# Kernel tuning notes

Hardware: AMD Instinct MI355X
Metric: run time of the kernel (lower is better)

The kernel has to match this reference:

```python
import jax, jax.numpy as jnp
import numpy as np

D_MODEL = 1024
NHEAD = 16
HEAD_DIM = D_MODEL // NHEAD
SCALE = 1.0 / np.sqrt(HEAD_DIM).astype(np.float32)
B, L = 2, 2048
NEG_INF = -1e30


def setup_inputs() -> dict:
    key = jax.random.key(0)
    ks = jax.random.split(key, 12)
    xav = np.sqrt(6.0 / (D_MODEL + D_MODEL)).astype(np.float32)  # xavier_uniform gain=1
    def lin_w(k):
        return jax.random.uniform(k, (D_MODEL, D_MODEL), jnp.float32, -xav, xav)
    x = jax.random.normal(ks[0], (B, L, D_MODEL), jnp.float32)
    role_mask = jax.random.randint(ks[1], (B, L), 0, 2, jnp.int32)
    # causal attention mask: True = masked (upper triangle above diagonal)
    attn_mask = jnp.triu(jnp.ones((L, L), jnp.bool_), k=1)
    # random key padding: True = padded key
    key_padding_mask = jax.random.randint(ks[2], (B, L), 0, 2, jnp.int32).astype(jnp.bool_)
    return {
        "x": x,
        "role_mask": role_mask,
        "attn_mask": attn_mask,
        "key_padding_mask": key_padding_mask,
        "Wq": lin_w(ks[3]), "bq": jnp.zeros((D_MODEL,), jnp.float32),
        "Wk": lin_w(ks[4]), "bk": jnp.zeros((D_MODEL,), jnp.float32),
        "Wv": lin_w(ks[5]), "bv": jnp.zeros((D_MODEL,), jnp.float32),
        "Wo": lin_w(ks[6]), "bo": jnp.zeros((D_MODEL,), jnp.float32),
        "delta": jnp.asarray(1.0, jnp.float32),
    }


def reference(x, role_mask, attn_mask, key_padding_mask,
              Wq, bq, Wk, bk, Wv, bv, Wo, bo, delta):
    Bb, Ll, Dd = x.shape
    def heads(t):  # [B,L,D] -> [B,H,L,hd]
        return t.reshape(Bb, Ll, NHEAD, HEAD_DIM).transpose(0, 2, 1, 3)
    Q = heads(x @ Wq.T + bq)
    K = heads(x @ Wk.T + bk)
    V = heads(x @ Wv.T + bv)
    scores = jnp.einsum('bhqd,bhkd->bhqk', Q, K) * SCALE  # [B,H,L,L]
    same_role = (role_mask[:, :, None] == role_mask[:, None, :])  # [B,L,L]
    scores = scores + (same_role.astype(scores.dtype) * delta)[:, None, :, :]
    scores = jnp.where(attn_mask[None, None, :, :], -jnp.inf, scores)
    scores = jnp.where(key_padding_mask[:, None, None, :], -jnp.inf, scores)
    attn = jax.nn.softmax(scores, axis=-1)
    attn = jnp.nan_to_num(attn, nan=0.0, posinf=0.0, neginf=0.0)
    out = jnp.einsum('bhqk,bhkd->bhqd', attn, V)
    out = out.transpose(0, 2, 1, 3).reshape(Bb, Ll, Dd)
    return out @ Wo.T + bo
```

## Files before the change

### kernel.cpp

```cpp
#include <hip/hip_runtime.h>
#include <hip/hip_bf16.h>

#define DM 1024
#define NH 16
#define HD 64
#define BB 2
#define LL 2048
#define BL (BB * LL)
#define SCALE 0.125f
#define NEG_BIG -1e30f
#define LOG2E 1.4426950408889634f
#define SC2 (SCALE * LOG2E)
#define FIXM 16.0f
#define SLOTB 8448
#define POOL0_SLOTS 960

typedef __bf16 bf16;
typedef __bf16 bf16x8 __attribute__((ext_vector_type(8)));
typedef __bf16 bf16x4 __attribute__((ext_vector_type(4)));
typedef float f32x4 __attribute__((ext_vector_type(4)));

static __device__ inline bf16x8 load8(const bf16* p) {
    return *reinterpret_cast<const bf16x8*>(p);
}

static __device__ inline float scrub(float x) {
    union { float f; unsigned u; } c; c.f = x;
    return ((c.u & 0x7F800000u) == 0x7F800000u) ? 0.f : x;
}

typedef __attribute__((address_space(1))) const unsigned char ga_t;
typedef __attribute__((address_space(3))) unsigned char ls_t;
static __device__ inline void gload_lds16(const void* g, void* l) {
    __builtin_amdgcn_global_load_lds((ga_t*)g, (ls_t*)l, 16, 0, 0);
}

__global__ __launch_bounds__(256) void prep_all(
    const float* __restrict__ x,
    const float* __restrict__ Wq, const float* __restrict__ Wk,
    const float* __restrict__ Wv, const float* __restrict__ Wo,
    bf16* __restrict__ xb, bf16* __restrict__ Wqb, bf16* __restrict__ Wkb,
    bf16* __restrict__ Wvb, bf16* __restrict__ Wob,
    const int* __restrict__ role, const void* __restrict__ kpad,
    const float* __restrict__ deltap,
    float* __restrict__ biasC, int* __restrict__ cntq, int* __restrict__ ipos,
    bf16* __restrict__ kwc)
{
    const int tid = threadIdx.x;
    const int gid = blockIdx.x;
    if (gid < 2048) {
        const float* src; bf16* dst; size_t base;
        if (gid < 1024) { src = x; dst = xb; base = (size_t)gid * 1024; }
        else {
            const int wsel = (gid - 1024) >> 8;
            src = (wsel == 0) ? Wq : (wsel == 1) ? Wk : (wsel == 2) ? Wv : Wo;
            dst = (wsel == 0) ? Wqb : (wsel == 1) ? Wkb : (wsel == 2) ? Wvb : Wob;
            base = (size_t)((gid - 1024) & 255) * 1024;
        }
#pragma unroll
        for (int it = 0; it < 4; it++) {
            const size_t i = base + it * 256 + tid;
            const f32x4 v = ((const f32x4*)src)[i];
            bf16x4 o;
            o[0] = (bf16)v[0]; o[1] = (bf16)v[1]; o[2] = (bf16)v[2]; o[3] = (bf16)v[3];
            ((bf16x4*)dst)[i] = o;
        }
        return;
    }
    const int b = gid - 2048;
    const unsigned char* kb = (const unsigned char*)kpad;
    int f3F = 0, fLow = 0, fOff = 0;
    for (int i = (tid & 63); i < BL; i += 64) {
        const unsigned char v = kb[i];
        if (v == 0x3F) f3F = 1;
        if ((i & 3) < 2 && v) fLow = 1;
        if ((i & 3) && v) fOff = 1;
    }
    const int mode = __any(f3F) ? (__any(fLow) ? 3 : 2) : (__any(fOff) ? 1 : 0);

    __shared__ int ssum[256];
    int loc[8]; int s = 0;
#pragma unroll
    for (int j = 0; j < 8; j++) {
        const int i = tid * 8 + j, idx = b * LL + i;
        const bool pad = (mode == 0) ? (((const int*)kpad)[idx] != 0)
                       : (mode == 1) ? (((const unsigned char*)kpad)[idx] != 0)
                       : (mode == 2) ? (((const float*)kpad)[idx] != 0.f)
                                     : (((const unsigned short*)kpad)[idx] != 0);
        loc[j] = pad ? 0 : 1; s += loc[j];
    }
    ssum[tid] = s; __syncthreads();
    for (int off = 1; off < 256; off <<= 1) {
        const int t = (tid >= off) ? ssum[tid - off] : 0;
        __syncthreads();
        ssum[tid] += t;
        __syncthreads();
    }
    const int nv = ssum[255];
    int run = ssum[tid] - s;
    const float d2 = scrub(deltap[0]) * LOG2E;
#pragma unroll
    for (int j = 0; j < 8; j++) {
        const int i = tid * 8 + j, idx = b * LL + i;
        const int inc = run + loc[j];
        cntq[idx] = inc;
        if (loc[j]) {
            const int cp = inc - 1;
            const int r = role[idx];
            biasC[b * LL + cp]      = -FIXM + ((r == 0) ? d2 : 0.f);
            biasC[BL + b * LL + cp] = -FIXM + ((r == 1) ? d2 : 0.f);
            ipos[b * LL + cp] = i;
        }
        run = inc;
    }
    for (int i = nv + tid; i < LL; i += 256) {
        biasC[b * LL + i] = NEG_BIG;
        biasC[BL + b * LL + i] = NEG_BIG;
    }
    const int roundv = (nv + 63) & ~63;
    const int nt = roundv - nv;
    bf16x8 z;
#pragma unroll
    for (int j = 0; j < 8; j++) z[j] = (bf16)0.f;
    for (int u = tid; u < nt * NH * 8; u += 256) {
        const int c8 = u & 7; const int t2 = u >> 3;
        const int h = t2 / nt; const int rr = nv + t2 % nt;
        *(bf16x8*)&kwc[(((size_t)(b * NH + h) * LL) + rr) * HD + c8 * 8] = z;
    }
}

__global__ __launch_bounds__(256) void qkv_bf16(
    const bf16* __restrict__ xb,
    const bf16* __restrict__ Wqb, const bf16* __restrict__ Wkb, const bf16* __restrict__ Wvb,
    const float* __restrict__ bq, const float* __restrict__ bk, const float* __restrict__ bv,
    bf16* __restrict__ qw, bf16* __restrict__ kwc, bf16* __restrict__ vwc,
    const int* __restrict__ ipos, const int* __restrict__ cntq)
{
    __shared__ bf16 As[2][128 * 32];
    __shared__ bf16 Bs[2][128 * 32];
    const int tid = threadIdx.x;
    const int lane = tid & 63, w = tid >> 6;
    const int wm = w >> 1, wn = w & 1;
    const int ln = lane & 15, quad = lane >> 4;

    const int lin = blockIdx.y * 32 + blockIdx.x;
    const int xcd = lin & 7;
    const int t = lin >> 3;
    const int mloc = t & 3;
    const int yy = t >> 2;
    const int mt = xcd * 4 + mloc;
    const int sel = yy >> 3;
    const int nloc0 = (yy & 7) * 128;

    int b = 0, cp0 = 0, nvb = 0, m0 = 0;
    if (sel == 0) {
        m0 = mt * 128;
    } else {
        b = mt >> 4;
        cp0 = (mt & 15) * 128;
        nvb = cntq[b * LL + LL - 1];
        if (cp0 >= nvb) return;
    }

    const bf16* Wb = (sel == 0) ? Wqb : ((sel == 1) ? Wkb : Wvb);
    const float* bias = (sel == 0) ? bq : ((sel == 1) ? bk : bv);
    bf16* dstw = (sel == 0) ? qw : ((sel == 1) ? kwc : vwc);

    const int rA = lane >> 2;
    const int cA = (lane & 3) * 8;

    const bf16* asrc[2];
    const bf16* bsrc[2];
#pragma unroll
    for (int s = 0; s < 2; s++) {
        const int r = s * 64 + w * 16 + rA;
        int grow;
        if (sel == 0) grow = m0 + r;
        else {
            const int cp = cp0 + r;
            grow = b * LL + ((cp < nvb) ? ipos[b * LL + cp] : 0);
        }
        asrc[s] = xb + (size_t)grow * DM + cA;
        bsrc[s] = Wb + (size_t)(nloc0 + s * 64 + w * 16 + rA) * DM + cA;
    }

#pragma unroll
    for (int s = 0; s < 2; s++) {
        const int r0 = s * 64 + w * 16;
        gload_lds16(asrc[s], &As[0][r0 * 32]);
        gload_lds16(bsrc[s], &Bs[0][r0 * 32]);
    }

    f32x4 acc[4][4] = {};
    int cur = 0;
    for (int k0 = 0; k0 < DM; k0 += 32) {
        if (k0 + 32 < DM) {
#pragma unroll
            for (int s = 0; s < 2; s++) {
                const int r0 = s * 64 + w * 16;
                gload_lds16(asrc[s] + k0 + 32, &As[cur ^ 1][r0 * 32]);
                gload_lds16(bsrc[s] + k0 + 32, &Bs[cur ^ 1][r0 * 32]);
            }
            asm volatile("s_waitcnt vmcnt(4)" ::: "memory");
        } else {
            asm volatile("s_waitcnt vmcnt(0)" ::: "memory");
        }
        __builtin_amdgcn_s_barrier();

        bf16x8 a[4], bfr[4];
#pragma unroll
        for (int mi = 0; mi < 4; mi++)
            a[mi] = *(bf16x8*)&As[cur][(wm * 64 + mi * 16 + ln) * 32 + quad * 8];
#pragma unroll
        for (int ni = 0; ni < 4; ni++)
            bfr[ni] = *(bf16x8*)&Bs[cur][(wn * 64 + ni * 16 + ln) * 32 + quad * 8];
#pragma unroll
        for (int mi = 0; mi < 4; mi++)
#pragma unroll
            for (int ni = 0; ni < 4; ni++)
                acc[mi][ni] = __builtin_amdgcn_mfma_f32_16x16x32_bf16(a[mi], bfr[ni], acc[mi][ni], 0, 0, 0);

        __builtin_amdgcn_s_barrier();
        cur ^= 1;
    }

#pragma unroll
    for (int mi = 0; mi < 4; mi++) {
#pragma unroll
        for (int i = 0; i < 4; i++) {
            const int rr = wm * 64 + mi * 16 + quad * 4 + i;
            int batch, drow; bool valid;
            if (sel == 0) {
                const int row = m0 + rr;
                batch = row >> 11; drow = row & (LL - 1); valid = true;
            } else {
                const int cp = cp0 + rr;
                batch = b; drow = cp; valid = (cp < nvb);
            }
#pragma unroll
            for (int ni = 0; ni < 4; ni++) {
                const int ncol = nloc0 + wn * 64 + ni * 16 + ln;
                const int hh = ncol >> 6, dd = ncol & 63;
                const bf16 v = (bf16)scrub(acc[mi][ni][i] + bias[ncol]);
                if (valid)
                    dstw[(((size_t)(batch * NH + hh) * LL) + drow) * HD + dd] = v;
            }
        }
    }
}

__global__ __launch_bounds__(256) void vtrans(
    const bf16* __restrict__ vwc, bf16* __restrict__ vtc, const int* __restrict__ cntq)
{
    __shared__ bf16 T[64][72];
    const int l0 = blockIdx.x * 64;
    const int bh = blockIdx.y;
    const int b = bh >> 4;
    const int nv = cntq[b * LL + LL - 1];
    if (l0 >= ((nv + 63) & ~63)) return;
    const int tid = threadIdx.x;
#pragma unroll
    for (int it = 0; it < 2; it++) {
        const int idx = it * 256 + tid;
        const int row = idx >> 3, c8 = (idx & 7) * 8;
        const int wc = (((c8 >> 3) ^ ((row >> 3) & 7))) * 8;
        bf16x8 val;
#pragma unroll
        for (int j = 0; j < 8; j++) val[j] = (bf16)0.f;
        if (l0 + row < nv) val = load8(vwc + ((size_t)bh * LL + l0 + row) * HD + c8);
        *(bf16x8*)&T[row][wc] = val;
    }
    __syncthreads();
#pragma unroll
    for (int it = 0; it < 2; it++) {
        const int idx = it * 256 + tid;
        const int dd = idx >> 3, pg = (idx & 7) * 8;
        bf16x8 o;
#pragma unroll
        for (int j = 0; j < 8; j++) {
            const int r = pg + j;
            o[j] = T[r][(dd & 7) + ((((dd >> 3) ^ ((r >> 3) & 7))) << 3)];
        }
        *(bf16x8*)(vtc + ((size_t)bh * HD + dd) * LL + l0 + pg) = o;
    }
}

__global__ __launch_bounds__(256) void attn_v14(
    const bf16* __restrict__ qw, const bf16* __restrict__ kwc, const bf16* __restrict__ vtc,
    const int* __restrict__ role, const float* __restrict__ biasC, const int* __restrict__ cntq,
    char* __restrict__ pool0, char* __restrict__ pool1,
    bf16* __restrict__ attn_out)
{
    const int lin = blockIdx.y * 60 + blockIdx.x;
    const int xcd = lin & 7;
    const int t = lin >> 3;
    const int xg = t % 60;
    const int g = t / 60;
    const int bh = g * 8 + xcd;

    int qb, c;
    if (xg < 24)      { qb = 31 - xg / 3; c = xg % 3; }
    else if (xg < 48) { qb = 23 - (xg - 24) / 2; c = (xg - 24) % 2; }
    else              { qb = 59 - xg; c = 0; }
    const int nch = (qb + 12) / 12;

    __shared__ bf16 Ks[2][2][64 * 32];
    __shared__ bf16 Vs[2][2][64 * 32];

    const int tid = threadIdx.x;
    const int lane = tid & 63, w = tid >> 6;
    const int col = lane & 15, quad = lane >> 4;
    const int h = bh & (NH - 1), b = bh >> 4;
    const int q0 = qb * 64 + w * 16;

    const bf16* qbase = qw + (size_t)((b * NH + h) * LL) * HD;
    const bf16* kbase = kwc + (size_t)((b * NH + h) * LL) * HD;
    const bf16* vbase = vtc + (size_t)((b * NH + h) * HD) * LL;
    const int* rrow = role + b * LL;

    const int srow = lane >> 2;
    const int sslot = w * 16 + srow;
    const int trueK = ((sslot >> 5) & 1) * 32 + ((sslot >> 2) & 3) * 8
                    + ((sslot >> 4) & 1) * 4 + (sslot & 3);
    const int swz = ((lane & 3) ^ ((lane >> 3) & 3)) * 8;
    const bf16* ksrc = kbase + (size_t)trueK * HD + swz;
    const bf16* vsrc = vbase + (size_t)(w * 16 + srow) * LL + swz;

    bf16x8 qf[2];
    qf[0] = load8(qbase + (size_t)(q0 + col) * HD + quad * 8);
    qf[1] = load8(qbase + (size_t)(q0 + col) * HD + 32 + quad * 8);

    bf16x8 ones;
#pragma unroll
    for (int j = 0; j < 8; j++) ones[j] = (bf16)1.0f;

    const int qabs = q0 + col;
    const int role_q = rrow[qabs];
    const int cnt_q = cntq[b * LL + qabs];
    const float* bp = biasC + (size_t)role_q * BL + b * LL;

    const int cb = cntq[b * LL + qb * 64 + 63];
    const int Tb = (cb + 63) >> 6;
    const int t0c = (c * Tb) / nch;
    const int t1c = ((c + 1) * Tb) / nch;

    f32x4 ol = {};
    f32x4 o[4] = {};

    if (t0c < t1c) {
        const int kp = t0c * 64;
#pragma unroll
        for (int st = 0; st < 2; st++)
            gload_lds16(ksrc + (size_t)kp * HD + st * 32, &Ks[0][st][w * 512]);
#pragma unroll
        for (int kh = 0; kh < 2; kh++)
            gload_lds16(vsrc + kp + kh * 32, &Vs[0][kh][w * 512]);
    }

    const int rs = (quad ^ ((col >> 1) & 3)) * 8;

    for (int kt = t0c; kt < t1c; kt++) {
        const int cur = (kt - t0c) & 1;
        __syncthreads();

        if (kt + 1 < t1c) {
            const int k1 = (kt + 1) * 64;
#pragma unroll
            for (int st = 0; st < 2; st++)
                gload_lds16(ksrc + (size_t)k1 * HD + st * 32, &Ks[cur ^ 1][st][w * 512]);
#pragma unroll
            for (int kh = 0; kh < 2; kh++)
                gload_lds16(vsrc + k1 + kh * 32, &Vs[cur ^ 1][kh][w * 512]);
        }

        const int k0 = kt * 64;

        f32x4 s[4] = {};
#pragma unroll
        for (int st = 0; st < 2; st++) {
#pragma unroll
            for (int ns = 0; ns < 4; ns++) {
                const bf16x8 kf = *(bf16x8*)&Ks[cur][st][(ns * 16 + col) * 32 + rs];
                s[ns] = __builtin_amdgcn_mfma_f32_16x16x32_bf16(kf, qf[st], s[ns], 0, 0, 0);
            }
        }

        bf16x8 pf[2];
#pragma unroll
        for (int ns = 0; ns < 4; ns++) {
            const int kb_ = k0 + ((ns >> 1) << 5) + (quad << 3) + ((ns & 1) << 2);
            const f32x4 bv4 = *(const f32x4*)&bp[kb_];
#pragma unroll
            for (int i = 0; i < 4; i++) {
                float sv = fmaf(s[ns][i], SC2, bv4[i]);
                if ((kb_ + i) >= cnt_q) sv = NEG_BIG;
                pf[ns >> 1][(ns & 1) * 4 + i] = (bf16)exp2f(sv);
            }
        }

#pragma unroll
        for (int ns = 0; ns < 4; ns++) {
#pragma unroll
            for (int kh = 0; kh < 2; kh++) {
                const bf16x8 vf = *(bf16x8*)&Vs[cur][kh][(ns * 16 + col) * 32 + rs];
                o[ns] = __builtin_amdgcn_mfma_f32_16x16x32_bf16(vf, pf[kh], o[ns], 0, 0, 0);
            }
        }
#pragma unroll
        for (int kh = 0; kh < 2; kh++)
            ol = __builtin_amdgcn_mfma_f32_16x16x32_bf16(ones, pf[kh], ol, 0, 0, 0);
    }

    if (nch == 1) {
        const float inv = (ol[0] > 0.f) ? 1.f / ol[0] : 0.f;
        bf16* orow = attn_out + ((size_t)(b * LL) + qabs) * DM + h * HD;
#pragma unroll
        for (int ns = 0; ns < 4; ns++) {
            bf16x4 ov;
#pragma unroll
            for (int i = 0; i < 4; i++) ov[i] = (bf16)scrub(o[ns][i] * inv);
            *(bf16x4*)&orow[ns * 16 + quad * 4] = ov;
        }
    } else {
        const int base = (qb <= 23) ? (qb - 12) * 2 : 24 + (qb - 24) * 3;
        const int slot = bh * 48 + base + c;
        char* ptr = (slot < POOL0_SLOTS) ? (pool0 + (size_t)slot * SLOTB)
                                         : (pool1 + (size_t)(slot - POOL0_SLOTS) * SLOTB);
        bf16* op = (bf16*)ptr;
        float* lp = (float*)(ptr + 8192);
        const int r = w * 16 + col;
        if (quad == 0) lp[r] = ol[0];
#pragma unroll
        for (int ns = 0; ns < 4; ns++) {
            bf16x4 ov;
#pragma unroll
            for (int i = 0; i < 4; i++) ov[i] = (bf16)scrub(o[ns][i]);
            *(bf16x4*)&op[r * 64 + ns * 16 + quad * 4] = ov;
        }
    }
}

__global__ __launch_bounds__(256) void combine(
    const char* __restrict__ pool0, const char* __restrict__ pool1,
    bf16* __restrict__ attn_out)
{
    const int qb = 12 + blockIdx.x;
    const int bh = blockIdx.y;
    const int h = bh & (NH - 1), b = bh >> 4;
    const int nch = (qb + 12) / 12;
    const int base = (qb <= 23) ? (qb - 12) * 2 : 24 + (qb - 24) * 3;

    const char* ptr[3];
    for (int c = 0; c < nch; c++) {
        const int slot = bh * 48 + base + c;
        ptr[c] = (slot < POOL0_SLOTS) ? (pool0 + (size_t)slot * SLOTB)
                                      : (pool1 + (size_t)(slot - POOL0_SLOTS) * SLOTB);
    }

    __shared__ float linv[64];
    const int tid = threadIdx.x;
    if (tid < 64) {
        float ls = 0.f;
        for (int c = 0; c < nch; c++) ls += ((const float*)(ptr[c] + 8192))[tid];
        linv[tid] = (ls > 0.f) ? 1.f / ls : 0.f;
    }
    __syncthreads();

    const int r = tid >> 2;
    const int d0 = (tid & 3) * 16;
    float acc[16] = {};
    for (int c = 0; c < nch; c++) {
        const bf16* op = (const bf16*)ptr[c];
#pragma unroll
        for (int half = 0; half < 2; half++) {
            const bf16x8 v = load8(op + r * 64 + d0 + half * 8);
#pragma unroll
            for (int j = 0; j < 8; j++) acc[half * 8 + j] += (float)v[j];
        }
    }
    const float inv = linv[r];
    bf16x8 outv[2];
#pragma unroll
    for (int half = 0; half < 2; half++)
#pragma unroll
        for (int j = 0; j < 8; j++)
            outv[half][j] = (bf16)scrub(acc[half * 8 + j] * inv);
    bf16* orow = attn_out + ((size_t)(b * LL) + qb * 64 + r) * DM + h * HD + d0;
    *(bf16x8*)orow = outv[0];
    *(bf16x8*)(orow + 8) = outv[1];
}

__global__ __launch_bounds__(256) void out_bf16(
    const bf16* __restrict__ A, const bf16* __restrict__ Wb,
    const float* __restrict__ bias, float* __restrict__ out)
{
    __shared__ bf16 As[128 * 32];
    __shared__ bf16 Bs[64 * 32];
    const int tid = threadIdx.x;
    const int lane = tid & 63, w = tid >> 6;
    const int ln = lane & 15, quad = lane >> 4;

    const int lin = blockIdx.y * 32 + blockIdx.x;
    const int xcd = lin & 7;
    const int t = lin >> 3;
    const int mloc = t & 3;
    const int n = t >> 2;
    const int m0 = (xcd * 4 + mloc) * 128;
    const int n0 = n * 64;

    const int rA = lane >> 2;
    const int cA = (lane & 3) * 8;

    f32x4 acc[2][4] = {};
    for (int k0 = 0; k0 < DM; k0 += 32) {
        __syncthreads();
#pragma unroll
        for (int s = 0; s < 2; s++) {
            const int r0 = s * 64 + w * 16;
            gload_lds16(A + (size_t)(m0 + r0 + rA) * DM + k0 + cA, &As[r0 * 32]);
        }
        gload_lds16(Wb + (size_t)(n0 + w * 16 + rA) * DM + k0 + cA, &Bs[w * 16 * 32]);
        __syncthreads();
        bf16x8 a[2], b[4];
#pragma unroll
        for (int mi = 0; mi < 2; mi++)
            a[mi] = *(bf16x8*)&As[(w * 32 + mi * 16 + ln) * 32 + quad * 8];
#pragma unroll
        for (int ni = 0; ni < 4; ni++)
            b[ni] = *(bf16x8*)&Bs[(ni * 16 + ln) * 32 + quad * 8];
#pragma unroll
        for (int mi = 0; mi < 2; mi++)
#pragma unroll
            for (int ni = 0; ni < 4; ni++)
                acc[mi][ni] = __builtin_amdgcn_mfma_f32_16x16x32_bf16(a[mi], b[ni], acc[mi][ni], 0, 0, 0);
    }
#pragma unroll
    for (int mi = 0; mi < 2; mi++) {
#pragma unroll
        for (int ni = 0; ni < 4; ni++) {
            const int ncol = n0 + ni * 16 + ln;
            const float bv_ = bias[ncol];
#pragma unroll
            for (int i = 0; i < 4; i++) {
                const int row = m0 + w * 32 + mi * 16 + quad * 4 + i;
                out[(size_t)row * DM + ncol] = scrub(acc[mi][ni][i] + bv_);
            }
        }
    }
}

extern "C" void kernel_launch(void* const* d_in, const int* in_sizes, int n_in,
                              void* d_out, int out_size, void* d_ws, size_t ws_size,
                              hipStream_t stream) {
    const float* x    = (const float*)d_in[0];
    const int*   role = (const int*)d_in[1];
    const void*  kpad = d_in[3];
    const float* Wq = (const float*)d_in[4];
    const float* bq = (const float*)d_in[5];
    const float* Wk = (const float*)d_in[6];
    const float* bk = (const float*)d_in[7];
    const float* Wv = (const float*)d_in[8];
    const float* bv = (const float*)d_in[9];
    const float* Wo = (const float*)d_in[10];
    const float* bo = (const float*)d_in[11];
    const float* dl = (const float*)d_in[12];

    char* ws = (char*)d_ws;
    bf16* qw   = (bf16*)(ws);
    bf16* kwc  = (bf16*)(ws + (size_t)(8u  << 20));
    bf16* Wqb  = (bf16*)(ws + (size_t)(16u << 20));
    bf16* Wkb  = (bf16*)(ws + (size_t)(18u << 20));
    bf16* Wvb  = (bf16*)(ws + (size_t)(20u << 20));
    char* pool0 = ws + (size_t)(16u << 20);
    bf16* vwc  = (bf16*)(ws + (size_t)(24u << 20));
    bf16* aw   = (bf16*)(ws + (size_t)(24u << 20));
    bf16* vtc  = (bf16*)(ws + (size_t)(32u << 20));
    bf16* xb   = (bf16*)(ws + (size_t)(40u << 20));
    char* pool1 = ws + (size_t)(40u << 20);
    float* biasC = (float*)(ws + (size_t)(48u << 20));
    int*   cntq  = (int*)(ws + (size_t)(48u << 20) + 32768);
    int*   ipos  = (int*)(ws + (size_t)(48u << 20) + 49152);
    bf16* Wob  = (bf16*)(ws + (size_t)(48u << 20) + 65536);
    float* out = (float*)d_out;

    prep_all<<<dim3(2050), dim3(256), 0, stream>>>(
        x, Wq, Wk, Wv, Wo, xb, Wqb, Wkb, Wvb, Wob,
        role, kpad, dl, biasC, cntq, ipos, kwc);
    qkv_bf16<<<dim3(32, 24), dim3(256), 0, stream>>>(
        xb, Wqb, Wkb, Wvb, bq, bk, bv, qw, kwc, vwc, ipos, cntq);
    vtrans<<<dim3(32, 32), dim3(256), 0, stream>>>(vwc, vtc, cntq);
    attn_v14<<<dim3(60, 32), dim3(256), 0, stream>>>(
        qw, kwc, vtc, role, biasC, cntq, pool0, pool1, aw);
    combine<<<dim3(20, 32), dim3(256), 0, stream>>>(pool0, pool1, aw);
    out_bf16<<<dim3(32, 16), dim3(256), 0, stream>>>(aw, Wob, bo, out);
}
```

Measured before the change: 217.3 us.

## Triple-buffer LDS prefetch in QKV and output projection GEMMs

The QKV projection GEMM moves from double to triple LDS buffering with a two-stage-ahead prefetch, and its vmcnt waits are adjusted to match. The output projection GEMM, which previously loaded synchronously with two __syncthreads per k-step, gets the same three-buffer async pipeline. Sched barriers keep the compiler from reordering LDS reads across the barriers. The aim is to hide global-load latency behind MFMA work, at the cost of more LDS per block and possibly lower occupancy.

```diff
diff --git a/kernel.cpp b/kernel.cpp
--- a/kernel.cpp
+++ b/kernel.cpp
@@ -136,8 +136,8 @@
     bf16* __restrict__ qw, bf16* __restrict__ kwc, bf16* __restrict__ vwc,
     const int* __restrict__ ipos, const int* __restrict__ cntq)
 {
-    __shared__ bf16 As[2][128 * 32];
-    __shared__ bf16 Bs[2][128 * 32];
+    __shared__ bf16 As[3][128 * 32];
+    __shared__ bf16 Bs[3][128 * 32];
     const int tid = threadIdx.x;
     const int lane = tid & 63, w = tid >> 6;
     const int wm = w >> 1, wn = w & 1;
@@ -190,22 +190,33 @@
         gload_lds16(asrc[s], &As[0][r0 * 32]);
         gload_lds16(bsrc[s], &Bs[0][r0 * 32]);
     }
+#pragma unroll
+    for (int s = 0; s < 2; s++) {
+        const int r0 = s * 64 + w * 16;
+        gload_lds16(asrc[s] + 32, &As[1][r0 * 32]);
+        gload_lds16(bsrc[s] + 32, &Bs[1][r0 * 32]);
+    }
 
     f32x4 acc[4][4] = {};
     int cur = 0;
-    for (int k0 = 0; k0 < DM; k0 += 32) {
-        if (k0 + 32 < DM) {
+    for (int kk = 0; kk < 32; ++kk) {
+        if (kk + 2 < 32) {
+            const int pf = (cur >= 1) ? cur - 1 : 2;
+            const int ko = (kk + 2) * 32;
 #pragma unroll
             for (int s = 0; s < 2; s++) {
                 const int r0 = s * 64 + w * 16;
-                gload_lds16(asrc[s] + k0 + 32, &As[cur ^ 1][r0 * 32]);
-                gload_lds16(bsrc[s] + k0 + 32, &Bs[cur ^ 1][r0 * 32]);
+                gload_lds16(asrc[s] + ko, &As[pf][r0 * 32]);
+                gload_lds16(bsrc[s] + ko, &Bs[pf][r0 * 32]);
             }
+            asm volatile("s_waitcnt vmcnt(8)" ::: "memory");
+        } else if (kk + 2 == 32) {
             asm volatile("s_waitcnt vmcnt(4)" ::: "memory");
         } else {
             asm volatile("s_waitcnt vmcnt(0)" ::: "memory");
         }
         __builtin_amdgcn_s_barrier();
+        __builtin_amdgcn_sched_barrier(0);
 
         bf16x8 a[4], bfr[4];
 #pragma unroll
@@ -220,8 +231,9 @@
             for (int ni = 0; ni < 4; ni++)
                 acc[mi][ni] = __builtin_amdgcn_mfma_f32_16x16x32_bf16(a[mi], bfr[ni], acc[mi][ni], 0, 0, 0);
 
+        __builtin_amdgcn_sched_barrier(0);
         __builtin_amdgcn_s_barrier();
-        cur ^= 1;
+        cur = (cur == 2) ? 0 : cur + 1;
     }
 
 #pragma unroll
@@ -494,8 +506,8 @@
     const bf16* __restrict__ A, const bf16* __restrict__ Wb,
     const float* __restrict__ bias, float* __restrict__ out)
 {
-    __shared__ bf16 As[128 * 32];
-    __shared__ bf16 Bs[64 * 32];
+    __shared__ bf16 As[3][128 * 32];
+    __shared__ bf16 Bs[3][64 * 32];
     const int tid = threadIdx.x;
     const int lane = tid & 63, w = tid >> 6;
     const int ln = lane & 15, quad = lane >> 4;
@@ -510,29 +522,56 @@
 
     const int rA = lane >> 2;
     const int cA = (lane & 3) * 8;
+    const bf16* asrc[2];
+#pragma unroll
+    for (int s = 0; s < 2; s++)
+        asrc[s] = A + (size_t)(m0 + s * 64 + w * 16 + rA) * DM + cA;
+    const bf16* bsrc = Wb + (size_t)(n0 + w * 16 + rA) * DM + cA;
+
+#pragma unroll
+    for (int s = 0; s < 2; s++)
+        gload_lds16(asrc[s], &As[0][(s * 64 + w * 16) * 32]);
+    gload_lds16(bsrc, &Bs[0][w * 16 * 32]);
+#pragma unroll
+    for (int s = 0; s < 2; s++)
+        gload_lds16(asrc[s] + 32, &As[1][(s * 64 + w * 16) * 32]);
+    gload_lds16(bsrc + 32, &Bs[1][w * 16 * 32]);
 
     f32x4 acc[2][4] = {};
-    for (int k0 = 0; k0 < DM; k0 += 32) {
-        __syncthreads();
-#pragma unroll
-        for (int s = 0; s < 2; s++) {
-            const int r0 = s * 64 + w * 16;
-            gload_lds16(A + (size_t)(m0 + r0 + rA) * DM + k0 + cA, &As[r0 * 32]);
-        }
-        gload_lds16(Wb + (size_t)(n0 + w * 16 + rA) * DM + k0 + cA, &Bs[w * 16 * 32]);
-        __syncthreads();
-        bf16x8 a[2], b[4];
+    int cur = 0;
+    for (int kk = 0; kk < 32; ++kk) {
+        if (kk + 2 < 32) {
+            const int pf = (cur >= 1) ? cur - 1 : 2;
+            const int ko = (kk + 2) * 32;
+#pragma unroll
+            for (int s = 0; s < 2; s++)
+                gload_lds16(asrc[s] + ko, &As[pf][(s * 64 + w * 16) * 32]);
+            gload_lds16(bsrc + ko, &Bs[pf][w * 16 * 32]);
+            asm volatile("s_waitcnt vmcnt(6)" ::: "memory");
+        } else if (kk + 2 == 32) {
+            asm volatile("s_waitcnt vmcnt(3)" ::: "memory");
+        } else {
+            asm volatile("s_waitcnt vmcnt(0)" ::: "memory");
+        }
+        __builtin_amdgcn_s_barrier();
+        __builtin_amdgcn_sched_barrier(0);
+
+        bf16x8 a[2], bfr[4];
 #pragma unroll
         for (int mi = 0; mi < 2; mi++)
-            a[mi] = *(bf16x8*)&As[(w * 32 + mi * 16 + ln) * 32 + quad * 8];
+            a[mi] = *(bf16x8*)&As[cur][(w * 32 + mi * 16 + ln) * 32 + quad * 8];
 #pragma unroll
         for (int ni = 0; ni < 4; ni++)
-            b[ni] = *(bf16x8*)&Bs[(ni * 16 + ln) * 32 + quad * 8];
+            bfr[ni] = *(bf16x8*)&Bs[cur][(ni * 16 + ln) * 32 + quad * 8];
 #pragma unroll
         for (int mi = 0; mi < 2; mi++)
 #pragma unroll
             for (int ni = 0; ni < 4; ni++)
-                acc[mi][ni] = __builtin_amdgcn_mfma_f32_16x16x32_bf16(a[mi], b[ni], acc[mi][ni], 0, 0, 0);
+                acc[mi][ni] = __builtin_amdgcn_mfma_f32_16x16x32_bf16(a[mi], bfr[ni], acc[mi][ni], 0, 0, 0);
+
+        __builtin_amdgcn_sched_barrier(0);
+        __builtin_amdgcn_s_barrier();
+        cur = (cur == 2) ? 0 : cur + 1;
     }
 #pragma unroll
     for (int mi = 0; mi < 2; mi++) {
```

After: 218.3 us. Within noise of the previous version (+0.5%).
